# Kernel tuning notes

Hardware: AMD Instinct MI355X
Metric: run time of the kernel (lower is better)

The kernel has to match this reference:

```python
import jax, jax.numpy as jnp
import numpy as np

N_NODES = 50000
N_EDGES = 1600000
D_FEAT = 128
ORDER = 2


def setup_inputs() -> dict:
    key = jax.random.key(0)
    k1, k2, k3, k4 = jax.random.split(key, 4)
    x = jax.random.normal(k1, (N_NODES, D_FEAT), dtype=jnp.float32)
    adj_row = jax.random.randint(k2, (N_EDGES,), 0, N_NODES, dtype=jnp.int32)
    adj_col = jax.random.randint(k3, (N_EDGES,), 0, N_NODES, dtype=jnp.int32)
    adj_vals = jax.random.uniform(k4, (N_EDGES,), dtype=jnp.float32)
    return {"x": x, "adj_row": adj_row, "adj_col": adj_col, "adj_vals": adj_vals}


def reference(x, adj_row, adj_col, adj_vals):
    # SGC propagation: x <- A @ x, repeated `order` times.
    # A is sparse COO: A[row, col] = vals; spmm(A, x)[i] = sum_e vals[e]*x[col[e]] into row[e].
    for _ in range(ORDER):
        msgs = adj_vals[:, None] * x[adj_col]          # [E, F] gathered messages
        x = jax.ops.segment_sum(msgs, adj_row, num_segments=N_NODES)  # [N, F]
    return x
```

## Files before the change

kernel.cpp:

```cpp
#include <hip/hip_runtime.h>
#include <hip/hip_fp16.h>

#define N_NODES 50000
#define N_EDGES 1600000
#define D_FEAT  128
#define NB      196
#define BCAP    8704
#define SPAIR_STRIDE (BCAP * 2)
#define S_OUT_CAP 9216
#define OVF_CAP  8192

#define P1_WGS   400
#define P1_ROUND 4096
#define P1_CAP   38

__device__ __forceinline__ unsigned short f2bf(float f) {
    union { float f; unsigned u; } v; v.f = f;
    unsigned r = v.u + 0x7fff + ((v.u >> 16) & 1);
    return (unsigned short)(r >> 16);
}
__device__ __forceinline__ float bf_lo(unsigned w) {
    union { unsigned u; float f; } v; v.u = w << 16; return v.f;
}
__device__ __forceinline__ float bf_hi(unsigned w) {
    union { unsigned u; float f; } v; v.u = w & 0xffff0000u; return v.f;
}

__global__ __launch_bounds__(256) void conv_kernel(
    const float2* __restrict__ xin, unsigned* __restrict__ xb,
    int* __restrict__ gcnt)
{
    if (blockIdx.x == 0 && threadIdx.x <= NB)
        gcnt[threadIdx.x] = 0;
    int t = blockIdx.x * blockDim.x + threadIdx.x;
    if (t < N_NODES * (D_FEAT / 2)) {
        float2 f = xin[t];
        xb[t] = ((unsigned)f2bf(f.y) << 16) | (unsigned)f2bf(f.x);
    }
}

__global__ __launch_bounds__(256) void p1_bin_kernel(
    const int* __restrict__ row, const int* __restrict__ col,
    const float* __restrict__ val,
    int* __restrict__ gcnt, uint2* __restrict__ sedge, uint2* __restrict__ ovf)
{
    __shared__ uint2    s_buf[NB * P1_CAP];
    __shared__ unsigned s_cnt[NB];
    __shared__ int      s_base[NB];

    int wg = blockIdx.x, t = threadIdx.x;
    int e0 = (int)((long)wg * N_EDGES / P1_WGS);
    int e1 = (int)((long)(wg + 1) * N_EDGES / P1_WGS);

    for (int rbase = e0; rbase < e1; rbase += P1_ROUND) {
        int rend = rbase + P1_ROUND; if (rend > e1) rend = e1;
        for (int i = t; i < NB; i += 256) s_cnt[i] = 0;
        __syncthreads();
        for (int e = rbase + t; e < rend; e += 256) {
            int r = row[e];
            int b = r >> 8;
            uint2 rec;
            rec.x = ((unsigned)r << 16) | (unsigned)col[e];
            rec.y = __float_as_uint(val[e]);
            unsigned pos = atomicAdd(&s_cnt[b], 1u);
            if (pos < P1_CAP) {
                s_buf[b * P1_CAP + pos] = rec;
            } else {
                int p = atomicAdd(&gcnt[b], 1);
                if (p < BCAP) sedge[(long)b * BCAP + p] = rec;
                else {
                    int q = atomicAdd(&gcnt[NB], 1);
                    if (q < OVF_CAP) ovf[q] = rec;
                }
            }
        }
        __syncthreads();
        if (t < NB) {
            int c = (int)s_cnt[t]; if (c > P1_CAP) c = P1_CAP;
            s_base[t] = (c > 0) ? atomicAdd(&gcnt[t], c) : 0;
        }
        __syncthreads();
        if (t < NB) {
            int c = (int)s_cnt[t]; if (c > P1_CAP) c = P1_CAP;
            int gb = s_base[t];
            for (int i = 0; i < c; ++i) {
                int p = gb + i;
                if (p < BCAP) sedge[(long)t * BCAP + p] = s_buf[t * P1_CAP + i];
                else {
                    int q = atomicAdd(&gcnt[NB], 1);
                    if (q < OVF_CAP) ovf[q] = s_buf[t * P1_CAP + i];
                }
            }
        }
        __syncthreads();
    }
}

__global__ __launch_bounds__(256) void p2_sort_kernel(
    const int* __restrict__ gcnt, const uint2* __restrict__ sedge,
    const uint2* __restrict__ ovf,
    unsigned* __restrict__ spair, int2* __restrict__ row_se)
{
    __shared__ unsigned s_out[S_OUT_CAP];
    __shared__ int s_cnt[256];
    __shared__ int s_cur[256];

    int b = blockIdx.x, t = threadIdx.x;
    int cnt = gcnt[b]; if (cnt > BCAP) cnt = BCAP;
    int ovn = gcnt[NB]; if (ovn > OVF_CAP) ovn = OVF_CAP;
    int row0 = b << 8;
    long sbase = (long)b * BCAP;

    s_cnt[t] = 0;
    __syncthreads();
    for (int i = t; i < cnt; i += 256) {
        int fr = (int)(sedge[sbase + i].x >> 16) - row0;
        atomicAdd(&s_cnt[fr], 1);
    }
    for (int i = t; i < ovn; i += 256) {
        int r = (int)(ovf[i].x >> 16);
        if ((r >> 8) == b) atomicAdd(&s_cnt[r - row0], 1);
    }
    __syncthreads();
    int orig = s_cnt[t];
    __syncthreads();
    for (int off = 1; off < 256; off <<= 1) {
        int u = (t >= off) ? s_cnt[t - off] : 0;
        __syncthreads();
        s_cnt[t] += u;
        __syncthreads();
    }
    int excl  = s_cnt[t] - orig;
    int total = s_cnt[255];
    int r = row0 + t;
    if (r < N_NODES) row_se[r] = make_int2(b * SPAIR_STRIDE + excl, orig);
    s_cur[t] = excl;
    __syncthreads();

    if (total <= S_OUT_CAP) {
        for (int i = t; i < cnt; i += 256) {
            uint2 rec = sedge[sbase + i];
            int fr = (int)(rec.x >> 16) - row0;
            int p = atomicAdd(&s_cur[fr], 1);
            unsigned short hv = __half_as_ushort(__float2half(__uint_as_float(rec.y)));
            s_out[p] = ((rec.x & 0xffffu) << 16) | (unsigned)hv;
        }
        for (int i = t; i < ovn; i += 256) {
            uint2 rec = ovf[i];
            int rr = (int)(rec.x >> 16);
            if ((rr >> 8) == b) {
                int p = atomicAdd(&s_cur[rr - row0], 1);
                unsigned short hv = __half_as_ushort(__float2half(__uint_as_float(rec.y)));
                s_out[p] = ((rec.x & 0xffffu) << 16) | (unsigned)hv;
            }
        }
        __syncthreads();
        for (int i = t; i < total; i += 256)
            spair[(long)b * SPAIR_STRIDE + i] = s_out[i];
    } else {
        for (int i = t; i < cnt; i += 256) {
            uint2 rec = sedge[sbase + i];
            int fr = (int)(rec.x >> 16) - row0;
            int p = atomicAdd(&s_cur[fr], 1);
            unsigned short hv = __half_as_ushort(__float2half(__uint_as_float(rec.y)));
            spair[(long)b * SPAIR_STRIDE + p] = ((rec.x & 0xffffu) << 16) | (unsigned)hv;
        }
    }
}

template <bool WRITE_BF16>
__global__ __launch_bounds__(256) void spmm_csr_bf2_kernel(
    const int2*     __restrict__ row_se,
    const unsigned* __restrict__ spair,
    const unsigned* __restrict__ xb,
    unsigned* __restrict__ outb,
    float*    __restrict__ outf)
{
    int wave = (blockIdx.x * blockDim.x + threadIdx.x) >> 6;
    int lane = threadIdx.x & 63;
    int half  = lane >> 5;
    int fl    = lane & 31;
    int hbase = lane & 32;
    int row   = wave * 2 + half;
    if (row >= N_NODES) return;

    const int4 s4 = ((const int4*)row_se)[wave];
    int mystart = half ? s4.z : s4.x;
    int myn     = half ? s4.w : s4.y;
    int nmax    = (s4.y > s4.w) ? s4.y : s4.w;

    float acc0 = 0.f, acc1 = 0.f, acc2 = 0.f, acc3 = 0.f;

    for (int base = 0; base < nmax; base += 32) {
        int idx = base + fl;
        unsigned rec = (idx < myn) ? spair[mystart + idx] : 0u;
        int   c = (int)(rec >> 16);
        float v = __half2float(__ushort_as_half((unsigned short)(rec & 0xffffu)));

        int steps = nmax - base; if (steps > 32) steps = 32;
        int j = 0;
        for (; j + 8 <= steps; j += 8) {
            int   cc[8];
            float vv[8];
            uint2 ww[8];
            #pragma unroll
            for (int k = 0; k < 8; ++k) {
                cc[k] = __shfl(c, hbase + j + k, 64);
                vv[k] = __shfl(v, hbase + j + k, 64);
            }
            #pragma unroll
            for (int k = 0; k < 8; ++k)
                ww[k] = *(const uint2*)(xb + (long)cc[k] * (D_FEAT / 2) + fl * 2);
            #pragma unroll
            for (int k = 0; k < 8; ++k) {
                acc0 += vv[k] * bf_lo(ww[k].x);
                acc1 += vv[k] * bf_hi(ww[k].x);
                acc2 += vv[k] * bf_lo(ww[k].y);
                acc3 += vv[k] * bf_hi(ww[k].y);
            }
        }
        for (; j < steps; ++j) {
            int   cj = __shfl(c, hbase + j, 64);
            float vj = __shfl(v, hbase + j, 64);
            uint2 w = *(const uint2*)(xb + (long)cj * (D_FEAT / 2) + fl * 2);
            acc0 += vj * bf_lo(w.x);
            acc1 += vj * bf_hi(w.x);
            acc2 += vj * bf_lo(w.y);
            acc3 += vj * bf_hi(w.y);
        }
    }

    if (WRITE_BF16) {
        uint2 w;
        w.x = ((unsigned)f2bf(acc1) << 16) | (unsigned)f2bf(acc0);
        w.y = ((unsigned)f2bf(acc3) << 16) | (unsigned)f2bf(acc2);
        *(uint2*)(outb + (long)row * (D_FEAT / 2) + fl * 2) = w;
    } else {
        *(float4*)(outf + (long)row * D_FEAT + fl * 4) =
            make_float4(acc0, acc1, acc2, acc3);
    }
}

__global__ __launch_bounds__(256) void spmm_atomic_kernel(
    const int* __restrict__ row, const int* __restrict__ col,
    const float* __restrict__ vals, const float* __restrict__ xin,
    float* __restrict__ xout)
{
    long tid   = (long)blockIdx.x * blockDim.x + threadIdx.x;
    int  edge  = (int)(tid >> 5);
    int  chunk = (int)(tid & 31);
    if (edge >= N_EDGES) return;
    int   r = row[edge];
    int   c = col[edge];
    float v = vals[edge];
    const float4 xv = ((const float4*)(xin + (long)c * D_FEAT))[chunk];
    float* dst = xout + (long)r * D_FEAT + chunk * 4;
    unsafeAtomicAdd(dst + 0, v * xv.x);
    unsafeAtomicAdd(dst + 1, v * xv.y);
    unsafeAtomicAdd(dst + 2, v * xv.z);
    unsafeAtomicAdd(dst + 3, v * xv.w);
}

static inline size_t align_up(size_t x, size_t a) { return (x + a - 1) & ~(a - 1); }

extern "C" void kernel_launch(void* const* d_in, const int* in_sizes, int n_in,
                              void* d_out, int out_size, void* d_ws, size_t ws_size,
                              hipStream_t stream) {
    const float* x        = (const float*)d_in[0];
    const int*   adj_row  = (const int*)d_in[1];
    const int*   adj_col  = (const int*)d_in[2];
    const float* adj_vals = (const float*)d_in[3];
    float*       out      = (float*)d_out;

    const size_t bf_bytes = (size_t)N_NODES * (D_FEAT / 2) * sizeof(unsigned);

    char*     ws      = (char*)d_ws;
    size_t    off     = 0;
    unsigned* xb      = (unsigned*)(ws + off); off = align_up(off + bf_bytes, 512);
    unsigned* tmpb    = (unsigned*)(ws + off); off = align_up(off + bf_bytes, 512);
    uint2*    sedge   = (uint2*)   (ws + off); off = align_up(off + (size_t)NB * BCAP * 8, 512);
    int2*     row_se  = (int2*)    (ws + off); off = align_up(off + (size_t)(NB * 256) * 8, 512);
    int*      gcnt    = (int*)     (ws + off); off = align_up(off + (NB + 1) * sizeof(int), 512);
    uint2*    ovf     = (uint2*)   (ws + off); off = align_up(off + (size_t)OVF_CAP * 8, 512);
    const size_t needed = off;

    unsigned* spair = (unsigned*)sedge;

    const int block = 256;

    if (ws_size >= needed) {
        int cgrid = (N_NODES * (D_FEAT / 2) + block - 1) / block;
        conv_kernel<<<cgrid, block, 0, stream>>>((const float2*)x, xb, gcnt);
        p1_bin_kernel<<<P1_WGS, block, 0, stream>>>(adj_row, adj_col, adj_vals,
                                                    gcnt, sedge, ovf);
        p2_sort_kernel<<<NB, block, 0, stream>>>(gcnt, sedge, ovf, spair, row_se);

        int nwaves = (N_NODES + 1) / 2;
        int ngrid  = (int)(((long)nwaves * 64 + block - 1) / block);
        spmm_csr_bf2_kernel<true><<<ngrid, block, 0, stream>>>(
            row_se, spair, xb, tmpb, (float*)nullptr);
        spmm_csr_bf2_kernel<false><<<ngrid, block, 0, stream>>>(
            row_se, spair, tmpb, (unsigned*)nullptr, out);
    } else {
        float* tmp = (float*)ws;
        const size_t feat_bytes = (size_t)N_NODES * D_FEAT * sizeof(float);
        hipMemsetAsync(tmp, 0, feat_bytes, stream);
        hipMemsetAsync(out, 0, feat_bytes, stream);
        long total_threads = (long)N_EDGES * 32;
        long grid = (total_threads + block - 1) / block;
        spmm_atomic_kernel<<<dim3((unsigned)grid), dim3(block), 0, stream>>>(
            adj_row, adj_col, adj_vals, x, tmp);
        spmm_atomic_kernel<<<dim3((unsigned)grid), dim3(block), 0, stream>>>(
            adj_row, adj_col, adj_vals, tmp, out);
    }
}
```

Before: 226.1 us.

## Sub-bucket each row's edges by column range to localize gathers

The sort stage now orders each row's edges by one of seven column buckets (col >> 13) and stores the per-bucket lengths as packed 8-bit fields in a wider per-row metadata record. The SpMM kernel walks the buckets in order, so waves running concurrently tend to gather from the same slice of the feature table, which should improve L2/MALL hit rates. The cost is extra padding iterations per bucket (max of two rows' bucket lengths), more loop overhead, 8x larger shared counters, and per-bucket lengths capped at 255 in 8-bit fields.

```diff
diff --git a/kernel.cpp b/kernel.cpp
--- a/kernel.cpp
+++ b/kernel.cpp
@@ -13,6 +13,9 @@
 #define P1_WGS   400
 #define P1_ROUND 4096
 #define P1_CAP   38
+
+#define NCB   7
+#define CBSH  13
 
 __device__ __forceinline__ unsigned short f2bf(float f) {
     union { float f; unsigned u; } v; v.f = f;
@@ -99,11 +102,11 @@
 __global__ __launch_bounds__(256) void p2_sort_kernel(
     const int* __restrict__ gcnt, const uint2* __restrict__ sedge,
     const uint2* __restrict__ ovf,
-    unsigned* __restrict__ spair, int2* __restrict__ row_se)
+    unsigned* __restrict__ spair, int4* __restrict__ row_meta)
 {
     __shared__ unsigned s_out[S_OUT_CAP];
-    __shared__ int s_cnt[256];
-    __shared__ int s_cur[256];
+    __shared__ int s_cnt[256 * 8];
+    __shared__ int s_sum[256];
 
     int b = blockIdx.x, t = threadIdx.x;
     int cnt = gcnt[b]; if (cnt > BCAP) cnt = BCAP;
@@ -111,37 +114,56 @@
     int row0 = b << 8;
     long sbase = (long)b * BCAP;
 
-    s_cnt[t] = 0;
+    for (int i = t; i < 256 * 8; i += 256) s_cnt[i] = 0;
     __syncthreads();
     for (int i = t; i < cnt; i += 256) {
-        int fr = (int)(sedge[sbase + i].x >> 16) - row0;
-        atomicAdd(&s_cnt[fr], 1);
+        unsigned rx = sedge[sbase + i].x;
+        int fr = (int)(rx >> 16) - row0;
+        int cb = (int)(rx & 0xffffu) >> CBSH;
+        atomicAdd(&s_cnt[(fr << 3) + cb], 1);
     }
     for (int i = t; i < ovn; i += 256) {
-        int r = (int)(ovf[i].x >> 16);
-        if ((r >> 8) == b) atomicAdd(&s_cnt[r - row0], 1);
+        unsigned rx = ovf[i].x;
+        int r = (int)(rx >> 16);
+        if ((r >> 8) == b)
+            atomicAdd(&s_cnt[((r - row0) << 3) + ((int)(rx & 0xffffu) >> CBSH)], 1);
     }
     __syncthreads();
-    int orig = s_cnt[t];
+
+    int l[8]; int tot = 0;
+    #pragma unroll
+    for (int k = 0; k < 8; ++k) { l[k] = s_cnt[(t << 3) + k]; tot += l[k]; }
+    s_sum[t] = tot;
     __syncthreads();
     for (int off = 1; off < 256; off <<= 1) {
-        int u = (t >= off) ? s_cnt[t - off] : 0;
-        __syncthreads();
-        s_cnt[t] += u;
-        __syncthreads();
-    }
-    int excl  = s_cnt[t] - orig;
-    int total = s_cnt[255];
+        int u = (t >= off) ? s_sum[t - off] : 0;
+        __syncthreads();
+        s_sum[t] += u;
+        __syncthreads();
+    }
+    int excl_row = s_sum[t] - tot;
+    int total    = s_sum[255];
+
+    int pre = 0;
+    #pragma unroll
+    for (int k = 0; k < 8; ++k) { s_cnt[(t << 3) + k] = excl_row + pre; pre += l[k]; }
     int r = row0 + t;
-    if (r < N_NODES) row_se[r] = make_int2(b * SPAIR_STRIDE + excl, orig);
-    s_cur[t] = excl;
+    if (r < N_NODES) {
+        int4 m;
+        m.x = b * SPAIR_STRIDE + excl_row;
+        m.y = (l[0]) | (l[1] << 8) | (l[2] << 16) | (l[3] << 24);
+        m.z = (l[4]) | (l[5] << 8) | (l[6] << 16);
+        m.w = tot;
+        row_meta[r] = m;
+    }
     __syncthreads();
 
     if (total <= S_OUT_CAP) {
         for (int i = t; i < cnt; i += 256) {
             uint2 rec = sedge[sbase + i];
             int fr = (int)(rec.x >> 16) - row0;
-            int p = atomicAdd(&s_cur[fr], 1);
+            int cb = (int)(rec.x & 0xffffu) >> CBSH;
+            int p = atomicAdd(&s_cnt[(fr << 3) + cb], 1);
             unsigned short hv = __half_as_ushort(__float2half(__uint_as_float(rec.y)));
             s_out[p] = ((rec.x & 0xffffu) << 16) | (unsigned)hv;
         }
@@ -149,7 +171,8 @@
             uint2 rec = ovf[i];
             int rr = (int)(rec.x >> 16);
             if ((rr >> 8) == b) {
-                int p = atomicAdd(&s_cur[rr - row0], 1);
+                int cb = (int)(rec.x & 0xffffu) >> CBSH;
+                int p = atomicAdd(&s_cnt[((rr - row0) << 3) + cb], 1);
                 unsigned short hv = __half_as_ushort(__float2half(__uint_as_float(rec.y)));
                 s_out[p] = ((rec.x & 0xffffu) << 16) | (unsigned)hv;
             }
@@ -161,7 +184,8 @@
         for (int i = t; i < cnt; i += 256) {
             uint2 rec = sedge[sbase + i];
             int fr = (int)(rec.x >> 16) - row0;
-            int p = atomicAdd(&s_cur[fr], 1);
+            int cb = (int)(rec.x & 0xffffu) >> CBSH;
+            int p = atomicAdd(&s_cnt[(fr << 3) + cb], 1);
             unsigned short hv = __half_as_ushort(__float2half(__uint_as_float(rec.y)));
             spair[(long)b * SPAIR_STRIDE + p] = ((rec.x & 0xffffu) << 16) | (unsigned)hv;
         }
@@ -170,7 +194,7 @@
 
 template <bool WRITE_BF16>
 __global__ __launch_bounds__(256) void spmm_csr_bf2_kernel(
-    const int2*     __restrict__ row_se,
+    const int4*     __restrict__ row_meta,
     const unsigned* __restrict__ spair,
     const unsigned* __restrict__ xb,
     unsigned* __restrict__ outb,
@@ -184,50 +208,60 @@
     int row   = wave * 2 + half;
     if (row >= N_NODES) return;
 
-    const int4 s4 = ((const int4*)row_se)[wave];
-    int mystart = half ? s4.z : s4.x;
-    int myn     = half ? s4.w : s4.y;
-    int nmax    = (s4.y > s4.w) ? s4.y : s4.w;
+    int4 mA = row_meta[wave * 2];
+    int4 mB = row_meta[wave * 2 + 1];
+    int mystart = half ? mB.x : mA.x;
+    unsigned long lensA = ((unsigned long)(unsigned)mA.z << 32) | (unsigned)mA.y;
+    unsigned long lensB = ((unsigned long)(unsigned)mB.z << 32) | (unsigned)mB.y;
 
     float acc0 = 0.f, acc1 = 0.f, acc2 = 0.f, acc3 = 0.f;
-
-    for (int base = 0; base < nmax; base += 32) {
-        int idx = base + fl;
-        unsigned rec = (idx < myn) ? spair[mystart + idx] : 0u;
-        int   c = (int)(rec >> 16);
-        float v = __half2float(__ushort_as_half((unsigned short)(rec & 0xffffu)));
-
-        int steps = nmax - base; if (steps > 32) steps = 32;
-        int j = 0;
-        for (; j + 8 <= steps; j += 8) {
-            int   cc[8];
-            float vv[8];
-            uint2 ww[8];
-            #pragma unroll
-            for (int k = 0; k < 8; ++k) {
-                cc[k] = __shfl(c, hbase + j + k, 64);
-                vv[k] = __shfl(v, hbase + j + k, 64);
-            }
-            #pragma unroll
-            for (int k = 0; k < 8; ++k)
-                ww[k] = *(const uint2*)(xb + (long)cc[k] * (D_FEAT / 2) + fl * 2);
-            #pragma unroll
-            for (int k = 0; k < 8; ++k) {
-                acc0 += vv[k] * bf_lo(ww[k].x);
-                acc1 += vv[k] * bf_hi(ww[k].x);
-                acc2 += vv[k] * bf_lo(ww[k].y);
-                acc3 += vv[k] * bf_hi(ww[k].y);
-            }
-        }
-        for (; j < steps; ++j) {
-            int   cj = __shfl(c, hbase + j, 64);
-            float vj = __shfl(v, hbase + j, 64);
-            uint2 w = *(const uint2*)(xb + (long)cj * (D_FEAT / 2) + fl * 2);
-            acc0 += vj * bf_lo(w.x);
-            acc1 += vj * bf_hi(w.x);
-            acc2 += vj * bf_lo(w.y);
-            acc3 += vj * bf_hi(w.y);
-        }
+    int offMy = 0;
+
+    for (int cb = 0; cb < NCB; ++cb) {
+        int lA = (int)((lensA >> (cb * 8)) & 0xffu);
+        int lB = (int)((lensB >> (cb * 8)) & 0xffu);
+        int steps = (lA > lB) ? lA : lB;
+        int myn   = half ? lB : lA;
+
+        for (int base = 0; base < steps; base += 32) {
+            int rem = steps - base; if (rem > 32) rem = 32;
+            int idx = base + fl;
+            unsigned rec = (idx < myn) ? spair[mystart + offMy + idx] : 0u;
+            int   c = (int)(rec >> 16);
+            float v = __half2float(__ushort_as_half((unsigned short)(rec & 0xffffu)));
+
+            int j = 0;
+            for (; j + 8 <= rem; j += 8) {
+                int   cc[8];
+                float vv[8];
+                uint2 ww[8];
+                #pragma unroll
+                for (int k = 0; k < 8; ++k) {
+                    cc[k] = __shfl(c, hbase + j + k, 64);
+                    vv[k] = __shfl(v, hbase + j + k, 64);
+                }
+                #pragma unroll
+                for (int k = 0; k < 8; ++k)
+                    ww[k] = *(const uint2*)(xb + (long)cc[k] * (D_FEAT / 2) + fl * 2);
+                #pragma unroll
+                for (int k = 0; k < 8; ++k) {
+                    acc0 += vv[k] * bf_lo(ww[k].x);
+                    acc1 += vv[k] * bf_hi(ww[k].x);
+                    acc2 += vv[k] * bf_lo(ww[k].y);
+                    acc3 += vv[k] * bf_hi(ww[k].y);
+                }
+            }
+            for (; j < rem; ++j) {
+                int   cj = __shfl(c, hbase + j, 64);
+                float vj = __shfl(v, hbase + j, 64);
+                uint2 w = *(const uint2*)(xb + (long)cj * (D_FEAT / 2) + fl * 2);
+                acc0 += vj * bf_lo(w.x);
+                acc1 += vj * bf_hi(w.x);
+                acc2 += vj * bf_lo(w.y);
+                acc3 += vj * bf_hi(w.y);
+            }
+        }
+        offMy += myn;
     }
 
     if (WRITE_BF16) {
@@ -279,7 +313,7 @@
     unsigned* xb      = (unsigned*)(ws + off); off = align_up(off + bf_bytes, 512);
     unsigned* tmpb    = (unsigned*)(ws + off); off = align_up(off + bf_bytes, 512);
     uint2*    sedge   = (uint2*)   (ws + off); off = align_up(off + (size_t)NB * BCAP * 8, 512);
-    int2*     row_se  = (int2*)    (ws + off); off = align_up(off + (size_t)(NB * 256) * 8, 512);
+    int4*     row_meta= (int4*)    (ws + off); off = align_up(off + (size_t)(NB * 256) * 16, 512);
     int*      gcnt    = (int*)     (ws + off); off = align_up(off + (NB + 1) * sizeof(int), 512);
     uint2*    ovf     = (uint2*)   (ws + off); off = align_up(off + (size_t)OVF_CAP * 8, 512);
     const size_t needed = off;
@@ -293,14 +327,14 @@
         conv_kernel<<<cgrid, block, 0, stream>>>((const float2*)x, xb, gcnt);
         p1_bin_kernel<<<P1_WGS, block, 0, stream>>>(adj_row, adj_col, adj_vals,
                                                     gcnt, sedge, ovf);
-        p2_sort_kernel<<<NB, block, 0, stream>>>(gcnt, sedge, ovf, spair, row_se);
+        p2_sort_kernel<<<NB, block, 0, stream>>>(gcnt, sedge, ovf, spair, row_meta);
 
         int nwaves = (N_NODES + 1) / 2;
         int ngrid  = (int)(((long)nwaves * 64 + block - 1) / block);
         spmm_csr_bf2_kernel<true><<<ngrid, block, 0, stream>>>(
-            row_se, spair, xb, tmpb, (float*)nullptr);
+            row_meta, spair, xb, tmpb, (float*)nullptr);
         spmm_csr_bf2_kernel<false><<<ngrid, block, 0, stream>>>(
-            row_se, spair, tmpb, (unsigned*)nullptr, out);
+            row_meta, spair, tmpb, (unsigned*)nullptr, out);
     } else {
         float* tmp = (float*)ws;
         const size_t feat_bytes = (size_t)N_NODES * D_FEAT * sizeof(float);
```

Measured after the change: 269.1 us. 1.19x slower.

## Replace two-pass bucket sort with direct per-row ELL binning via global atomics

Applied to the files above, without the earlier changes.

Drops the two-phase bucketed binning and counting sort that built a CSR layout, and replaces it with a single kernel that does a global atomicAdd per row counter and writes packed (col, fp16 val) records into a fixed-width ELL slot array of width 64. The SpMM kernels read each row's ELL slots directly and then scan a small overflow list for rows with more than 64 edges. This removes one launch and the shared-memory sort passes, but adds heavy global atomic contention on 50k counters and scattered writes. It also makes every wave loop over the whole overflow count, which is expected to be near zero for these inputs with about 32 edges per row on average.

```diff
diff --git a/kernel.cpp b/kernel.cpp
--- a/kernel.cpp
+++ b/kernel.cpp
@@ -4,15 +4,8 @@
 #define N_NODES 50000
 #define N_EDGES 1600000
 #define D_FEAT  128
-#define NB      196
-#define BCAP    8704
-#define SPAIR_STRIDE (BCAP * 2)
-#define S_OUT_CAP 9216
-#define OVF_CAP  8192
-
-#define P1_WGS   400
-#define P1_ROUND 4096
-#define P1_CAP   38
+#define ELL_W   64
+#define OVF_CAP 8192
 
 __device__ __forceinline__ unsigned short f2bf(float f) {
     union { float f; unsigned u; } v; v.f = f;
@@ -28,150 +21,43 @@
 
 __global__ __launch_bounds__(256) void conv_kernel(
     const float2* __restrict__ xin, unsigned* __restrict__ xb,
-    int* __restrict__ gcnt)
-{
-    if (blockIdx.x == 0 && threadIdx.x <= NB)
-        gcnt[threadIdx.x] = 0;
+    int* __restrict__ cnt)
+{
     int t = blockIdx.x * blockDim.x + threadIdx.x;
+    if (t <= N_NODES) cnt[t] = 0;
     if (t < N_NODES * (D_FEAT / 2)) {
         float2 f = xin[t];
         xb[t] = ((unsigned)f2bf(f.y) << 16) | (unsigned)f2bf(f.x);
     }
 }
 
-__global__ __launch_bounds__(256) void p1_bin_kernel(
+__global__ __launch_bounds__(256) void bin_kernel(
     const int* __restrict__ row, const int* __restrict__ col,
     const float* __restrict__ val,
-    int* __restrict__ gcnt, uint2* __restrict__ sedge, uint2* __restrict__ ovf)
-{
-    __shared__ uint2    s_buf[NB * P1_CAP];
-    __shared__ unsigned s_cnt[NB];
-    __shared__ int      s_base[NB];
-
-    int wg = blockIdx.x, t = threadIdx.x;
-    int e0 = (int)((long)wg * N_EDGES / P1_WGS);
-    int e1 = (int)((long)(wg + 1) * N_EDGES / P1_WGS);
-
-    for (int rbase = e0; rbase < e1; rbase += P1_ROUND) {
-        int rend = rbase + P1_ROUND; if (rend > e1) rend = e1;
-        for (int i = t; i < NB; i += 256) s_cnt[i] = 0;
-        __syncthreads();
-        for (int e = rbase + t; e < rend; e += 256) {
-            int r = row[e];
-            int b = r >> 8;
-            uint2 rec;
-            rec.x = ((unsigned)r << 16) | (unsigned)col[e];
-            rec.y = __float_as_uint(val[e]);
-            unsigned pos = atomicAdd(&s_cnt[b], 1u);
-            if (pos < P1_CAP) {
-                s_buf[b * P1_CAP + pos] = rec;
-            } else {
-                int p = atomicAdd(&gcnt[b], 1);
-                if (p < BCAP) sedge[(long)b * BCAP + p] = rec;
-                else {
-                    int q = atomicAdd(&gcnt[NB], 1);
-                    if (q < OVF_CAP) ovf[q] = rec;
-                }
-            }
-        }
-        __syncthreads();
-        if (t < NB) {
-            int c = (int)s_cnt[t]; if (c > P1_CAP) c = P1_CAP;
-            s_base[t] = (c > 0) ? atomicAdd(&gcnt[t], c) : 0;
-        }
-        __syncthreads();
-        if (t < NB) {
-            int c = (int)s_cnt[t]; if (c > P1_CAP) c = P1_CAP;
-            int gb = s_base[t];
-            for (int i = 0; i < c; ++i) {
-                int p = gb + i;
-                if (p < BCAP) sedge[(long)t * BCAP + p] = s_buf[t * P1_CAP + i];
-                else {
-                    int q = atomicAdd(&gcnt[NB], 1);
-                    if (q < OVF_CAP) ovf[q] = s_buf[t * P1_CAP + i];
-                }
-            }
-        }
-        __syncthreads();
-    }
-}
-
-__global__ __launch_bounds__(256) void p2_sort_kernel(
-    const int* __restrict__ gcnt, const uint2* __restrict__ sedge,
-    const uint2* __restrict__ ovf,
-    unsigned* __restrict__ spair, int2* __restrict__ row_se)
-{
-    __shared__ unsigned s_out[S_OUT_CAP];
-    __shared__ int s_cnt[256];
-    __shared__ int s_cur[256];
-
-    int b = blockIdx.x, t = threadIdx.x;
-    int cnt = gcnt[b]; if (cnt > BCAP) cnt = BCAP;
-    int ovn = gcnt[NB]; if (ovn > OVF_CAP) ovn = OVF_CAP;
-    int row0 = b << 8;
-    long sbase = (long)b * BCAP;
-
-    s_cnt[t] = 0;
-    __syncthreads();
-    for (int i = t; i < cnt; i += 256) {
-        int fr = (int)(sedge[sbase + i].x >> 16) - row0;
-        atomicAdd(&s_cnt[fr], 1);
-    }
-    for (int i = t; i < ovn; i += 256) {
-        int r = (int)(ovf[i].x >> 16);
-        if ((r >> 8) == b) atomicAdd(&s_cnt[r - row0], 1);
-    }
-    __syncthreads();
-    int orig = s_cnt[t];
-    __syncthreads();
-    for (int off = 1; off < 256; off <<= 1) {
-        int u = (t >= off) ? s_cnt[t - off] : 0;
-        __syncthreads();
-        s_cnt[t] += u;
-        __syncthreads();
-    }
-    int excl  = s_cnt[t] - orig;
-    int total = s_cnt[255];
-    int r = row0 + t;
-    if (r < N_NODES) row_se[r] = make_int2(b * SPAIR_STRIDE + excl, orig);
-    s_cur[t] = excl;
-    __syncthreads();
-
-    if (total <= S_OUT_CAP) {
-        for (int i = t; i < cnt; i += 256) {
-            uint2 rec = sedge[sbase + i];
-            int fr = (int)(rec.x >> 16) - row0;
-            int p = atomicAdd(&s_cur[fr], 1);
-            unsigned short hv = __half_as_ushort(__float2half(__uint_as_float(rec.y)));
-            s_out[p] = ((rec.x & 0xffffu) << 16) | (unsigned)hv;
-        }
-        for (int i = t; i < ovn; i += 256) {
-            uint2 rec = ovf[i];
-            int rr = (int)(rec.x >> 16);
-            if ((rr >> 8) == b) {
-                int p = atomicAdd(&s_cur[rr - row0], 1);
-                unsigned short hv = __half_as_ushort(__float2half(__uint_as_float(rec.y)));
-                s_out[p] = ((rec.x & 0xffffu) << 16) | (unsigned)hv;
-            }
-        }
-        __syncthreads();
-        for (int i = t; i < total; i += 256)
-            spair[(long)b * SPAIR_STRIDE + i] = s_out[i];
+    int* __restrict__ cnt, unsigned* __restrict__ ell, uint2* __restrict__ ovf)
+{
+    int e = blockIdx.x * blockDim.x + threadIdx.x;
+    if (e >= N_EDGES) return;
+    int   r = row[e];
+    int   c = col[e];
+    float v = val[e];
+    int pos = atomicAdd(&cnt[r], 1);
+    unsigned short hv = __half_as_ushort(__float2half(v));
+    unsigned rec = ((unsigned)c << 16) | (unsigned)hv;
+    if (pos < ELL_W) {
+        ell[(long)r * ELL_W + pos] = rec;
     } else {
-        for (int i = t; i < cnt; i += 256) {
-            uint2 rec = sedge[sbase + i];
-            int fr = (int)(rec.x >> 16) - row0;
-            int p = atomicAdd(&s_cur[fr], 1);
-            unsigned short hv = __half_as_ushort(__float2half(__uint_as_float(rec.y)));
-            spair[(long)b * SPAIR_STRIDE + p] = ((rec.x & 0xffffu) << 16) | (unsigned)hv;
-        }
+        int q = atomicAdd(&cnt[N_NODES], 1);
+        if (q < OVF_CAP) { ovf[q].x = ((unsigned)r << 16) | (unsigned)c;
+                           ovf[q].y = __float_as_uint(v); }
     }
 }
 
 template <bool WRITE_BF16>
-__global__ __launch_bounds__(256) void spmm_csr_bf2_kernel(
-    const int2*     __restrict__ row_se,
-    const unsigned* __restrict__ spair,
+__global__ __launch_bounds__(256) void spmm_ell_kernel(
+    const int*      __restrict__ cnt,
+    const unsigned* __restrict__ ell,
+    const uint2*    __restrict__ ovf,
     const unsigned* __restrict__ xb,
     unsigned* __restrict__ outb,
     float*    __restrict__ outf)
@@ -184,16 +70,18 @@
     int row   = wave * 2 + half;
     if (row >= N_NODES) return;
 
-    const int4 s4 = ((const int4*)row_se)[wave];
-    int mystart = half ? s4.z : s4.x;
-    int myn     = half ? s4.w : s4.y;
-    int nmax    = (s4.y > s4.w) ? s4.y : s4.w;
+    int2 c2 = ((const int2*)cnt)[wave];
+    int nA = c2.x > ELL_W ? ELL_W : c2.x;
+    int nB = c2.y > ELL_W ? ELL_W : c2.y;
+    int myn  = half ? nB : nA;
+    int nmax = (nA > nB) ? nA : nB;
+    long mybase = (long)row * ELL_W;
 
     float acc0 = 0.f, acc1 = 0.f, acc2 = 0.f, acc3 = 0.f;
 
     for (int base = 0; base < nmax; base += 32) {
         int idx = base + fl;
-        unsigned rec = (idx < myn) ? spair[mystart + idx] : 0u;
+        unsigned rec = (idx < myn) ? ell[mybase + idx] : 0u;
         int   c = (int)(rec >> 16);
         float v = __half2float(__ushort_as_half((unsigned short)(rec & 0xffffu)));
 
@@ -230,6 +118,21 @@
         }
     }
 
+    int ovn = cnt[N_NODES]; if (ovn > OVF_CAP) ovn = OVF_CAP;
+    for (int k = 0; k < ovn; ++k) {
+        uint2 rec = ovf[k];
+        int rr = (int)(rec.x >> 16);
+        if (rr == row) {
+            int   cc = (int)(rec.x & 0xffffu);
+            float v  = __uint_as_float(rec.y);
+            uint2 w = *(const uint2*)(xb + (long)cc * (D_FEAT / 2) + fl * 2);
+            acc0 += v * bf_lo(w.x);
+            acc1 += v * bf_hi(w.x);
+            acc2 += v * bf_lo(w.y);
+            acc3 += v * bf_hi(w.y);
+        }
+    }
+
     if (WRITE_BF16) {
         uint2 w;
         w.x = ((unsigned)f2bf(acc1) << 16) | (unsigned)f2bf(acc0);
@@ -278,29 +181,27 @@
     size_t    off     = 0;
     unsigned* xb      = (unsigned*)(ws + off); off = align_up(off + bf_bytes, 512);
     unsigned* tmpb    = (unsigned*)(ws + off); off = align_up(off + bf_bytes, 512);
-    uint2*    sedge   = (uint2*)   (ws + off); off = align_up(off + (size_t)NB * BCAP * 8, 512);
-    int2*     row_se  = (int2*)    (ws + off); off = align_up(off + (size_t)(NB * 256) * 8, 512);
-    int*      gcnt    = (int*)     (ws + off); off = align_up(off + (NB + 1) * sizeof(int), 512);
+    unsigned* ell     = (unsigned*)(ws + off); off = align_up(off + (size_t)N_NODES * ELL_W * 4, 512);
+    int*      cnt     = (int*)     (ws + off); off = align_up(off + (size_t)(N_NODES + 1) * 4, 512);
     uint2*    ovf     = (uint2*)   (ws + off); off = align_up(off + (size_t)OVF_CAP * 8, 512);
     const size_t needed = off;
 
-    unsigned* spair = (unsigned*)sedge;
-
     const int block = 256;
 
     if (ws_size >= needed) {
         int cgrid = (N_NODES * (D_FEAT / 2) + block - 1) / block;
-        conv_kernel<<<cgrid, block, 0, stream>>>((const float2*)x, xb, gcnt);
-        p1_bin_kernel<<<P1_WGS, block, 0, stream>>>(adj_row, adj_col, adj_vals,
-                                                    gcnt, sedge, ovf);
-        p2_sort_kernel<<<NB, block, 0, stream>>>(gcnt, sedge, ovf, spair, row_se);
+        conv_kernel<<<cgrid, block, 0, stream>>>((const float2*)x, xb, cnt);
+
+        int bgrid = (N_EDGES + block - 1) / block;
+        bin_kernel<<<bgrid, block, 0, stream>>>(adj_row, adj_col, adj_vals,
+                                                cnt, ell, ovf);
 
         int nwaves = (N_NODES + 1) / 2;
         int ngrid  = (int)(((long)nwaves * 64 + block - 1) / block);
-        spmm_csr_bf2_kernel<true><<<ngrid, block, 0, stream>>>(
-            row_se, spair, xb, tmpb, (float*)nullptr);
-        spmm_csr_bf2_kernel<false><<<ngrid, block, 0, stream>>>(
-            row_se, spair, tmpb, (unsigned*)nullptr, out);
+        spmm_ell_kernel<true><<<ngrid, block, 0, stream>>>(
+            cnt, ell, ovf, xb, tmpb, (float*)nullptr);
+        spmm_ell_kernel<false><<<ngrid, block, 0, stream>>>(
+            cnt, ell, ovf, tmpb, (unsigned*)nullptr, out);
     } else {
         float* tmp = (float*)ws;
         const size_t feat_bytes = (size_t)N_NODES * D_FEAT * sizeof(float);
```

Measured after the change: 292.1 us. +29.2%, slower.

## Fuse sort and both SpMM passes into one cooperative kernel with grid syncs

Applied to the files above, without the earlier changes.

Merges the per-bucket sort and the two CSR SpMM propagation passes into a single cooperative kernel, separated by grid-wide barriers, and widens the sort blocks from 256 to 1024 threads. The aim is to remove two kernel launch boundaries and the tail idle time between dependent stages. In exchange, the fused kernel runs fewer resident waves in a grid-stride loop and pays for grid syncs. A fallback to the separate kernels remains if the cooperative launch is unavailable.

```diff
diff --git a/kernel.cpp b/kernel.cpp
--- a/kernel.cpp
+++ b/kernel.cpp
@@ -1,5 +1,8 @@
 #include <hip/hip_runtime.h>
 #include <hip/hip_fp16.h>
+#include <hip/hip_cooperative_groups.h>
+
+namespace cg = cooperative_groups;
 
 #define N_NODES 50000
 #define N_EDGES 1600000
@@ -9,6 +12,7 @@
 #define SPAIR_STRIDE (BCAP * 2)
 #define S_OUT_CAP 9216
 #define OVF_CAP  8192
+#define NWAVES  (N_NODES / 2)
 
 #define P1_WGS   400
 #define P1_ROUND 4096
@@ -96,56 +100,55 @@
     }
 }
 
-__global__ __launch_bounds__(256) void p2_sort_kernel(
+__device__ __forceinline__ void p2_block(
+    int b, int t,
     const int* __restrict__ gcnt, const uint2* __restrict__ sedge,
     const uint2* __restrict__ ovf,
-    unsigned* __restrict__ spair, int2* __restrict__ row_se)
-{
-    __shared__ unsigned s_out[S_OUT_CAP];
-    __shared__ int s_cnt[256];
-    __shared__ int s_cur[256];
-
-    int b = blockIdx.x, t = threadIdx.x;
+    unsigned* __restrict__ spair, int2* __restrict__ row_se,
+    unsigned* s_out, int* s_cnt, int* s_cur)
+{
     int cnt = gcnt[b]; if (cnt > BCAP) cnt = BCAP;
     int ovn = gcnt[NB]; if (ovn > OVF_CAP) ovn = OVF_CAP;
     int row0 = b << 8;
     long sbase = (long)b * BCAP;
 
-    s_cnt[t] = 0;
-    __syncthreads();
-    for (int i = t; i < cnt; i += 256) {
+    if (t < 256) s_cnt[t] = 0;
+    __syncthreads();
+    for (int i = t; i < cnt; i += 1024) {
         int fr = (int)(sedge[sbase + i].x >> 16) - row0;
         atomicAdd(&s_cnt[fr], 1);
     }
-    for (int i = t; i < ovn; i += 256) {
+    for (int i = t; i < ovn; i += 1024) {
         int r = (int)(ovf[i].x >> 16);
         if ((r >> 8) == b) atomicAdd(&s_cnt[r - row0], 1);
     }
     __syncthreads();
-    int orig = s_cnt[t];
+    int orig = (t < 256) ? s_cnt[t] : 0;
     __syncthreads();
     for (int off = 1; off < 256; off <<= 1) {
-        int u = (t >= off) ? s_cnt[t - off] : 0;
-        __syncthreads();
-        s_cnt[t] += u;
-        __syncthreads();
-    }
-    int excl  = s_cnt[t] - orig;
+        int u = (t >= off && t < 256) ? s_cnt[t - off] : 0;
+        __syncthreads();
+        if (t < 256) s_cnt[t] += u;
+        __syncthreads();
+    }
     int total = s_cnt[255];
-    int r = row0 + t;
-    if (r < N_NODES) row_se[r] = make_int2(b * SPAIR_STRIDE + excl, orig);
-    s_cur[t] = excl;
+    if (t < 256) {
+        int excl = s_cnt[t] - orig;
+        int r = row0 + t;
+        if (r < N_NODES) row_se[r] = make_int2(b * SPAIR_STRIDE + excl, orig);
+        s_cur[t] = excl;
+    }
     __syncthreads();
 
     if (total <= S_OUT_CAP) {
-        for (int i = t; i < cnt; i += 256) {
+        for (int i = t; i < cnt; i += 1024) {
             uint2 rec = sedge[sbase + i];
             int fr = (int)(rec.x >> 16) - row0;
             int p = atomicAdd(&s_cur[fr], 1);
             unsigned short hv = __half_as_ushort(__float2half(__uint_as_float(rec.y)));
             s_out[p] = ((rec.x & 0xffffu) << 16) | (unsigned)hv;
         }
-        for (int i = t; i < ovn; i += 256) {
+        for (int i = t; i < ovn; i += 1024) {
             uint2 rec = ovf[i];
             int rr = (int)(rec.x >> 16);
             if ((rr >> 8) == b) {
@@ -155,10 +158,10 @@
             }
         }
         __syncthreads();
-        for (int i = t; i < total; i += 256)
+        for (int i = t; i < total; i += 1024)
             spair[(long)b * SPAIR_STRIDE + i] = s_out[i];
     } else {
-        for (int i = t; i < cnt; i += 256) {
+        for (int i = t; i < cnt; i += 1024) {
             uint2 rec = sedge[sbase + i];
             int fr = (int)(rec.x >> 16) - row0;
             int p = atomicAdd(&s_cur[fr], 1);
@@ -166,23 +169,34 @@
             spair[(long)b * SPAIR_STRIDE + p] = ((rec.x & 0xffffu) << 16) | (unsigned)hv;
         }
     }
+    __syncthreads();
+}
+
+__global__ __launch_bounds__(1024) void p2_sort_kernel(
+    const int* __restrict__ gcnt, const uint2* __restrict__ sedge,
+    const uint2* __restrict__ ovf,
+    unsigned* __restrict__ spair, int2* __restrict__ row_se)
+{
+    __shared__ unsigned s_out[S_OUT_CAP];
+    __shared__ int s_cnt[256];
+    __shared__ int s_cur[256];
+    p2_block(blockIdx.x, threadIdx.x, gcnt, sedge, ovf, spair, row_se,
+             s_out, s_cnt, s_cur);
 }
 
 template <bool WRITE_BF16>
-__global__ __launch_bounds__(256) void spmm_csr_bf2_kernel(
+__device__ __forceinline__ void spmm_wave(
+    int wave, int lane,
     const int2*     __restrict__ row_se,
     const unsigned* __restrict__ spair,
     const unsigned* __restrict__ xb,
     unsigned* __restrict__ outb,
     float*    __restrict__ outf)
 {
-    int wave = (blockIdx.x * blockDim.x + threadIdx.x) >> 6;
-    int lane = threadIdx.x & 63;
     int half  = lane >> 5;
     int fl    = lane & 31;
     int hbase = lane & 32;
     int row   = wave * 2 + half;
-    if (row >= N_NODES) return;
 
     const int4 s4 = ((const int4*)row_se)[wave];
     int mystart = half ? s4.z : s4.x;
@@ -239,6 +253,52 @@
         *(float4*)(outf + (long)row * D_FEAT + fl * 4) =
             make_float4(acc0, acc1, acc2, acc3);
     }
+}
+
+template <bool WRITE_BF16>
+__global__ __launch_bounds__(256) void spmm_csr_bf2_kernel(
+    const int2*     __restrict__ row_se,
+    const unsigned* __restrict__ spair,
+    const unsigned* __restrict__ xb,
+    unsigned* __restrict__ outb,
+    float*    __restrict__ outf)
+{
+    int wave = (blockIdx.x * blockDim.x + threadIdx.x) >> 6;
+    if (wave >= NWAVES) return;
+    spmm_wave<WRITE_BF16>(wave, threadIdx.x & 63, row_se, spair, xb, outb, outf);
+}
+
+__global__ __launch_bounds__(1024) void fused_p2_spmm_kernel(
+    const int* __restrict__ gcnt, const uint2* __restrict__ sedge,
+    const uint2* __restrict__ ovf,
+    unsigned* __restrict__ spair, int2* __restrict__ row_se,
+    const unsigned* __restrict__ xb,
+    unsigned* __restrict__ tmpb, float* __restrict__ outf)
+{
+    __shared__ unsigned s_out[S_OUT_CAP];
+    __shared__ int s_cnt[256];
+    __shared__ int s_cur[256];
+
+    for (int b = blockIdx.x; b < NB; b += gridDim.x)
+        p2_block(b, threadIdx.x, gcnt, sedge, ovf, spair, row_se,
+                 s_out, s_cnt, s_cur);
+
+    __threadfence();
+    cg::this_grid().sync();
+
+    int wib  = threadIdx.x >> 6;
+    int lane = threadIdx.x & 63;
+    int gw   = blockIdx.x * (1024 >> 6) + wib;
+    int strd = gridDim.x * (1024 >> 6);
+
+    for (int w = gw; w < NWAVES; w += strd)
+        spmm_wave<true>(w, lane, row_se, spair, xb, tmpb, (float*)nullptr);
+
+    __threadfence();
+    cg::this_grid().sync();
+
+    for (int w = gw; w < NWAVES; w += strd)
+        spmm_wave<false>(w, lane, row_se, spair, tmpb, (unsigned*)nullptr, outf);
 }
 
 __global__ __launch_bounds__(256) void spmm_atomic_kernel(
@@ -293,14 +353,34 @@
         conv_kernel<<<cgrid, block, 0, stream>>>((const float2*)x, xb, gcnt);
         p1_bin_kernel<<<P1_WGS, block, 0, stream>>>(adj_row, adj_col, adj_vals,
                                                     gcnt, sedge, ovf);
-        p2_sort_kernel<<<NB, block, 0, stream>>>(gcnt, sedge, ovf, spair, row_se);
-
-        int nwaves = (N_NODES + 1) / 2;
-        int ngrid  = (int)(((long)nwaves * 64 + block - 1) / block);
-        spmm_csr_bf2_kernel<true><<<ngrid, block, 0, stream>>>(
-            row_se, spair, xb, tmpb, (float*)nullptr);
-        spmm_csr_bf2_kernel<false><<<ngrid, block, 0, stream>>>(
-            row_se, spair, tmpb, (unsigned*)nullptr, out);
+
+        static int coop_blocks = -1;
+        if (coop_blocks < 0) {
+            int nb = 0;
+            hipError_t qe = hipOccupancyMaxActiveBlocksPerMultiprocessor(
+                &nb, fused_p2_spmm_kernel, 1024, 0);
+            if (qe != hipSuccess || nb < 0) nb = 0;
+            coop_blocks = nb * 256;
+            if (coop_blocks > 512) coop_blocks = 512;
+        }
+        bool did_coop = false;
+        if (coop_blocks >= 256) {
+            void* args[] = {(void*)&gcnt, (void*)&sedge, (void*)&ovf,
+                            (void*)&spair, (void*)&row_se, (void*)&xb,
+                            (void*)&tmpb, (void*)&out};
+            hipError_t e = hipLaunchCooperativeKernel(
+                (const void*)fused_p2_spmm_kernel,
+                dim3((unsigned)coop_blocks), dim3(1024), args, 0, stream);
+            did_coop = (e == hipSuccess);
+        }
+        if (!did_coop) {
+            p2_sort_kernel<<<NB, 1024, 0, stream>>>(gcnt, sedge, ovf, spair, row_se);
+            int ngrid = (int)(((long)NWAVES * 64 + block - 1) / block);
+            spmm_csr_bf2_kernel<true><<<ngrid, block, 0, stream>>>(
+                row_se, spair, xb, tmpb, (float*)nullptr);
+            spmm_csr_bf2_kernel<false><<<ngrid, block, 0, stream>>>(
+                row_se, spair, tmpb, (unsigned*)nullptr, out);
+        }
     } else {
         float* tmp = (float*)ws;
         const size_t feat_bytes = (size_t)N_NODES * D_FEAT * sizeof(float);
```

Measured after the change: 215.1 us. 1.05x faster.
